# Performance work log

Measured on AMD Instinct MI355X. Metric: run time of the kernel, lower is better.

Reference implementation:

```python
import jax, jax.numpy as jnp
import numpy as np


def conv3d(x, w, b=None):
    # x: (N,C,D,H,W), w: (O,I,3,3,3), stride 1, padding 1 == SAME
    y = jax.lax.conv_general_dilated(x, w, (1, 1, 1), 'SAME',
                                     dimension_numbers=('NCDHW', 'OIDHW', 'NCDHW'))
    if b is not None:
        y = y + b[None, :, None, None, None]
    return y


def grid_sample_3d(vol, gx, gy, gz):
    # vol: (B,D,H,W); gx/gy/gz: normalized coords in [-1,1], shape (B,D,H,W)
    # trilinear, zeros padding, align_corners=True (old torch default)
    B, D, H, W = vol.shape
    ix = (gx + 1.0) * 0.5 * (W - 1)
    iy = (gy + 1.0) * 0.5 * (H - 1)
    iz = (gz + 1.0) * 0.5 * (D - 1)
    x0f, y0f, z0f = jnp.floor(ix), jnp.floor(iy), jnp.floor(iz)
    tx, ty, tz = ix - x0f, iy - y0f, iz - z0f
    x0 = x0f.astype(jnp.int32)
    y0 = y0f.astype(jnp.int32)
    z0 = z0f.astype(jnp.int32)
    vol_flat = vol.reshape(B, D * H * W)
    out = jnp.zeros_like(vol)
    for dz in (0, 1):
        for dy in (0, 1):
            for dx in (0, 1):
                xc, yc, zc = x0 + dx, y0 + dy, z0 + dz
                w = ((tx if dx else 1.0 - tx) * (ty if dy else 1.0 - ty)
                     * (tz if dz else 1.0 - tz))
                inb = ((xc >= 0) & (xc < W) & (yc >= 0) & (yc < H)
                       & (zc >= 0) & (zc < D))
                idx = ((jnp.clip(zc, 0, D - 1) * H + jnp.clip(yc, 0, H - 1)) * W
                       + jnp.clip(xc, 0, W - 1))
                val = jnp.take_along_axis(vol_flat, idx.reshape(B, -1), axis=1)
                val = val.reshape(B, D, H, W) * inb.astype(vol.dtype)
                out = out + w * val
    return out


def setup_inputs() -> dict:
    key = jax.random.key(0)
    k1, k2, k3, k4 = jax.random.split(key, 4)
    B, C, Cout, S = 2, 32, 64, 64
    x = jax.random.normal(k1, (B, C, S, S, S), dtype=jnp.float32)
    w_off = jax.random.normal(k2, (3 * C, C, 3, 3, 3), dtype=jnp.float32) * 0.0005
    w_reg = jax.random.normal(k3, (Cout, C, 3, 3, 3), dtype=jnp.float32) * 0.05
    b_reg = jax.random.normal(k4, (Cout,), dtype=jnp.float32) * 0.05
    return {"x": x, "w_off": w_off, "w_reg": w_reg, "b_reg": b_reg}


def reference(x, w_off, w_reg, b_reg):
    B, C, D, H, W = x.shape
    offset = conv3d(x, w_off)  # (B, 3C, D, H, W)
    off_w, off_h, _ = jnp.split(offset, 3, axis=1)
    # NOTE: original code has offset_d = offset_h (faithful bug)
    off_d = off_h
    off_w = off_w.reshape(B * C, D, H, W)
    off_h = off_h.reshape(B * C, D, H, W)
    off_d = off_d.reshape(B * C, D, H, W)
    # np.meshgrid default 'xy' indexing: shapes (H, W, D) -> requires D==H==W
    gw, gh, gd = np.meshgrid(np.linspace(-1, 1, W), np.linspace(-1, 1, H),
                             np.linspace(-1, 1, D))
    grid_w = jnp.asarray(gw, dtype=x.dtype)
    grid_h = jnp.asarray(gh, dtype=x.dtype)
    grid_d = jnp.asarray(gd, dtype=x.dtype)
    off_w = off_w + grid_w
    off_h = off_h + grid_h
    off_d = off_d + grid_d
    vol = x.reshape(B * C, D, H, W)
    # torch grid stack order: (offset_h, offset_w, offset_d) -> (x, y, z)
    sampled = grid_sample_3d(vol, off_h, off_w, off_d)
    sampled = sampled.reshape(B, C, D, H, W)
    return conv3d(sampled, w_reg, b_reg)
```

## Files before the change

kernel.cpp:

```cpp
#include <hip/hip_runtime.h>
#include <cstddef>

#define S 64
#define VOL (64*64*64)
#define CIN 32

typedef __attribute__((ext_vector_type(8))) short bf16x8;
typedef __attribute__((ext_vector_type(4))) float floatx4;

struct __attribute__((packed, aligned(4))) fpair { float x, y; };

__device__ __forceinline__ unsigned short f2bf(float f) {
    union { float f; unsigned u; } v; v.f = f;
    unsigned r = v.u + 0x7fffu + ((v.u >> 16) & 1u);
    return (unsigned short)(r >> 16);
}
__device__ __forceinline__ float bf2f(unsigned short h) {
    union { unsigned u; float f; } v; v.u = ((unsigned)h) << 16;
    return v.f;
}
__device__ __forceinline__ int iclamp(int v, int lo, int hi) {
    return v < lo ? lo : (v > hi ? hi : v);
}

__device__ __forceinline__ void load4bf(const float* p, unsigned short* o) {
    const float4 v = *(const float4*)p;
    o[0] = f2bf(v.x); o[1] = f2bf(v.y); o[2] = f2bf(v.z); o[3] = f2bf(v.w);
}
__device__ __forceinline__ void load4bf(const unsigned short* p, unsigned short* o) {
    const ushort4 v = *(const ushort4*)p;
    o[0] = v.x; o[1] = v.y; o[2] = v.z; o[3] = v.w;
}

__global__ void prep_w_kernel(const float* __restrict__ w_off,
                              const float* __restrict__ w_reg,
                              unsigned short* __restrict__ wt1,
                              unsigned short* __restrict__ wt2) {
    int i = blockIdx.x * 256 + threadIdx.x;
    if (i >= 27 * 64 * 32) return;
    int ci = i & 31;
    int co = (i >> 5) & 63;
    int tap = i >> 11;
    wt1[i] = f2bf(w_off[(co * 32 + ci) * 27 + tap]);
    wt2[i] = f2bf(w_reg[(co * 32 + ci) * 27 + tap]);
}

template <typename TIN, bool WRITE_OFF>
__global__ __launch_bounds__(256, 2)
void conv_mfma_kernel(const TIN* __restrict__ src,
                      const unsigned short* __restrict__ wt,
                      const float* __restrict__ bias,
                      void* __restrict__ dstv) {
    __shared__ unsigned short lds[16 * 64 * 32];

    const int d0 = blockIdx.x * 2;
    const int h0 = blockIdx.y * 2;
    const int b  = blockIdx.z;
    const int t  = threadIdx.x;

    const TIN* sb = src + (size_t)b * CIN * VOL;

    const int w0 = (t & 15) << 2;
    const int c0 = (t >> 4) << 1;
    const int jj = c0 >> 3;
    const int cb = (c0 & 7) << 1;
    const int sw01 = (w0 >> 1) & 3;
    const int sw23 = ((w0 >> 1) + 1) & 3;

#pragma unroll
    for (int rr = 0; rr < 16; ++rr) {
        const int z = d0 - 1 + (rr >> 2);
        const int y = h0 - 1 + (rr & 3);
        unsigned pk0 = 0, pk1 = 0, pk2 = 0, pk3 = 0;
        if (((unsigned)z < 64u) && ((unsigned)y < 64u)) {
            const TIN* p0 = sb + (size_t)c0 * VOL + (z * 64 + y) * 64 + w0;
            unsigned short va[4], vb[4];
            load4bf(p0, va);
            load4bf(p0 + VOL, vb);
            pk0 = (unsigned)va[0] | ((unsigned)vb[0] << 16);
            pk1 = (unsigned)va[1] | ((unsigned)vb[1] << 16);
            pk2 = (unsigned)va[2] | ((unsigned)vb[2] << 16);
            pk3 = (unsigned)va[3] | ((unsigned)vb[3] << 16);
        }
        char* rbase = (char*)lds + (rr << 12) + cb;
        *(unsigned*)(rbase + ((w0 + 0) << 6) + ((jj ^ sw01) << 4)) = pk0;
        *(unsigned*)(rbase + ((w0 + 1) << 6) + ((jj ^ sw01) << 4)) = pk1;
        *(unsigned*)(rbase + ((w0 + 2) << 6) + ((jj ^ sw23) << 4)) = pk2;
        *(unsigned*)(rbase + ((w0 + 3) << 6) + ((jj ^ sw23) << 4)) = pk3;
    }
    __syncthreads();

    const int lane = t & 63;
    const int wv   = t >> 6;
    const int r    = lane & 15;
    const int q    = lane >> 4;
    const int dd   = wv >> 1;
    const int hh   = wv & 1;

    int P[4][3];
#pragma unroll
    for (int nt = 0; nt < 4; ++nt)
#pragma unroll
        for (int kw = 0; kw < 3; ++kw) {
            const int s  = nt * 16 + r + kw - 1;
            const int sc = s & 63;
            P[nt][kw] = (sc << 6) + ((q ^ ((sc >> 1) & 3)) << 4);
        }

    floatx4 acc[4][4];
#pragma unroll
    for (int mt = 0; mt < 4; ++mt)
#pragma unroll
        for (int nt = 0; nt < 4; ++nt)
#pragma unroll
            for (int rg = 0; rg < 4; ++rg) acc[mt][nt][rg] = 0.f;

    const bf16x8 z8 = {0, 0, 0, 0, 0, 0, 0, 0};

#pragma unroll
    for (int tap = 0; tap < 27; ++tap) {
        const int kd = tap / 9;
        const int kh = (tap % 9) / 3;
        const int kw = tap % 3;
        const int rowb = ((((dd + kd) << 2) + hh + kh) << 12);

        bf16x8 afr[4];
#pragma unroll
        for (int mt = 0; mt < 4; ++mt)
            afr[mt] = *(const bf16x8*)&wt[tap * 2048 + (mt * 16 + r) * 32 + q * 8];

        bf16x8 bfr[4];
#pragma unroll
        for (int nt = 0; nt < 4; ++nt)
            bfr[nt] = *(const bf16x8*)((const char*)lds + rowb + P[nt][kw]);

        if (kw == 0) { if (r == 0)  bfr[0] = z8; }
        if (kw == 2) { if (r == 15) bfr[3] = z8; }

#pragma unroll
        for (int mt = 0; mt < 4; ++mt)
#pragma unroll
            for (int nt = 0; nt < 4; ++nt)
                acc[mt][nt] = __builtin_amdgcn_mfma_f32_16x16x32_bf16(
                                  afr[mt], bfr[nt], acc[mt][nt], 0, 0, 0);
    }

    const int dw = (d0 + dd) * 4096 + (h0 + hh) * 64;
    if (WRITE_OFF) {
#pragma unroll
        for (int mt = 0; mt < 2; ++mt) {
#pragma unroll
            for (int nt = 0; nt < 4; ++nt) {
#pragma unroll
                for (int rg = 0; rg < 4; ++rg) {
                    const int c   = mt * 16 + q * 4 + rg;
                    const int pos = dw + nt * 16 + r;
                    const unsigned pk = (unsigned)f2bf(acc[mt][nt][rg])
                                      | ((unsigned)f2bf(acc[mt + 2][nt][rg]) << 16);
                    ((unsigned*)dstv)[((size_t)(b * 32 + c)) * VOL + pos] = pk;
                }
            }
        }
    } else {
#pragma unroll
        for (int mt = 0; mt < 4; ++mt) {
#pragma unroll
            for (int nt = 0; nt < 4; ++nt) {
#pragma unroll
                for (int rg = 0; rg < 4; ++rg) {
                    const int co  = mt * 16 + q * 4 + rg;
                    const int pos = dw + nt * 16 + r;
                    ((float*)dstv)[((size_t)(b * 64 + co)) * VOL + pos]
                        = acc[mt][nt][rg] + bias[co];
                }
            }
        }
    }
}

__global__ __launch_bounds__(256)
void gather_kernel(const float* __restrict__ x,
                   const unsigned* __restrict__ off32,
                   unsigned short* __restrict__ sampled) {
    __shared__ unsigned ostage[16][17];
    __shared__ float res[16][17];

    const unsigned gid = blockIdx.x;
    const int xcd = gid & 7;
    const int j   = gid >> 3;
    const int v   = xcd + ((j >> 10) << 3);
    const int bx  = j & 1023;
    const int c   = v & 31;
    const int b   = v >> 5;
    const int wt4 = bx & 3;
    const int dt  = (bx >> 2) & 3;
    const int h   = bx >> 4;
    const int t   = threadIdx.x;

    {
        const int wA = t & 15, dA = t >> 4;
        ostage[dA][wA] = off32[((size_t)(b * 32 + c)) * VOL
                               + (dt * 16 + dA) * 4096 + h * 64 + wt4 * 16 + wA];
    }
    __syncthreads();

    const int d_i = t & 15;
    const int w_i = t >> 4;
    const int d = dt * 16 + d_i;
    const int w = wt4 * 16 + w_i;

    const unsigned ow = ostage[d_i][w_i];
    const float offw = bf2f((unsigned short)(ow & 0xffffu));
    const float offh = bf2f((unsigned short)(ow >> 16));

    const float* vol = x + ((size_t)(b * CIN + c)) * VOL;

    const float ix = offh * 31.5f + (float)d;
    const float iy = offw * 31.5f + (float)h;
    const float iz = offh * 31.5f + (float)w;

    const float x0f = floorf(ix), y0f = floorf(iy), z0f = floorf(iz);
    const float tx = ix - x0f, ty = iy - y0f, tz = iz - z0f;
    const int ix0 = (int)x0f, iy0 = (int)y0f, iz0 = (int)z0f;

    const int bx0 = iclamp(ix0, 0, 62);
    const bool sel = (ix0 == bx0);
    const float w0x = ((unsigned)ix0 < 64u)       ? (1.f - tx) : 0.f;
    const float w1x = ((unsigned)(ix0 + 1) < 64u) ? tx         : 0.f;

    float out = 0.f;
#pragma unroll
    for (int dz = 0; dz < 2; ++dz) {
        const int zc = iz0 + dz;
        const bool zok = ((unsigned)zc < 64u);
        const int zcc = iclamp(zc, 0, 63);
        const float wz = dz ? tz : 1.f - tz;
#pragma unroll
        for (int dy = 0; dy < 2; ++dy) {
            const int yc = iy0 + dy;
            const bool yok = ((unsigned)yc < 64u);
            const int ycc = iclamp(yc, 0, 63);
            const float wzy = (zok && yok) ? wz * (dy ? ty : 1.f - ty) : 0.f;

            const fpair vp = *(const fpair*)&vol[(zcc * 64 + ycc) * 64 + bx0];
            const float v0 = sel ? vp.x : vp.y;
            const float v1 = sel ? vp.y : vp.x;
            out += wzy * (w0x * v0 + w1x * v1);
        }
    }

    res[w_i][d_i] = out;
    __syncthreads();

    const int w_o = t & 15;
    const int d_o = t >> 4;
    sampled[((size_t)(b * CIN + c)) * VOL + (dt * 16 + d_o) * 4096 + h * 64
            + wt4 * 16 + w_o] = f2bf(res[w_o][d_o]);
}

extern "C" void kernel_launch(void* const* d_in, const int* in_sizes, int n_in,
                              void* d_out, int out_size, void* d_ws, size_t ws_size,
                              hipStream_t stream) {
    (void)in_sizes; (void)n_in; (void)out_size; (void)ws_size;
    const float* x     = (const float*)d_in[0];
    const float* w_off = (const float*)d_in[1];
    const float* w_reg = (const float*)d_in[2];
    const float* b_reg = (const float*)d_in[3];
    float* out = (float*)d_out;

    unsigned* off32         = (unsigned*)d_ws;
    unsigned short* sampled = (unsigned short*)(off32 + (size_t)2 * 32 * VOL);
    unsigned short* wt1     = sampled + (size_t)2 * CIN * VOL;
    unsigned short* wt2     = wt1 + 27 * 64 * 32;

    prep_w_kernel<<<216, 256, 0, stream>>>(w_off, w_reg, wt1, wt2);

    dim3 cgrid(32, 32, 2);
    conv_mfma_kernel<float, true><<<cgrid, 256, 0, stream>>>(x, wt1, nullptr, (void*)off32);

    gather_kernel<<<65536, 256, 0, stream>>>(x, off32, sampled);

    conv_mfma_kernel<unsigned short, false><<<cgrid, 256, 0, stream>>>(sampled, wt2, b_reg, (void*)out);
}
```

Before: 426.2 us.

## Switch intermediates to channel-last bf16 layout with direct global-to-LDS loads

Adds a prepack kernel that converts x into a channel-last bf16 buffer, so both convolutions stage their input tiles with global_load_lds 16-byte transfers instead of strided per-channel loads and in-register packing. The offset conv now writes its output channel-last with 16-byte stores. The gather kernel has each thread handle all 32 channels of one voxel, which removes its LDS transposes and lets the sampled buffer reuse the prepacked buffer. This adds an extra pass over x and puts a 32-float array per gather thread, which raises register pressure. The gather's random reads are no longer grouped by channel per block, so cache locality may get worse.

```diff
diff --git a/kernel.cpp b/kernel.cpp
--- a/kernel.cpp
+++ b/kernel.cpp
@@ -23,13 +23,10 @@
     return v < lo ? lo : (v > hi ? hi : v);
 }
 
-__device__ __forceinline__ void load4bf(const float* p, unsigned short* o) {
-    const float4 v = *(const float4*)p;
-    o[0] = f2bf(v.x); o[1] = f2bf(v.y); o[2] = f2bf(v.z); o[3] = f2bf(v.w);
-}
-__device__ __forceinline__ void load4bf(const unsigned short* p, unsigned short* o) {
-    const ushort4 v = *(const ushort4*)p;
-    o[0] = v.x; o[1] = v.y; o[2] = v.z; o[3] = v.w;
+__device__ __forceinline__ void gload_lds16(const void* g, void* l) {
+    __builtin_amdgcn_global_load_lds(
+        (const __attribute__((address_space(1))) void*)g,
+        (__attribute__((address_space(3))) void*)l, 16, 0, 0);
 }
 
 __global__ void prep_w_kernel(const float* __restrict__ w_off,
@@ -45,9 +42,30 @@
     wt2[i] = f2bf(w_reg[(co * 32 + ci) * 27 + tap]);
 }
 
-template <typename TIN, bool WRITE_OFF>
+__global__ __launch_bounds__(256)
+void prepack_kernel(const float* __restrict__ x, unsigned* __restrict__ xb) {
+    const unsigned id = blockIdx.x * 256 + threadIdx.x;
+    const int b   = id >> 18;
+    const int pos = id & (VOL - 1);
+    const float* sp = x + (size_t)b * 32 * VOL + pos;
+    float v[32];
+#pragma unroll
+    for (int c = 0; c < 32; ++c) v[c] = sp[(size_t)c * VOL];
+    unsigned* dp = xb + (size_t)id * 16;
+#pragma unroll
+    for (int i = 0; i < 4; ++i) {
+        uint4 pk;
+        pk.x = (unsigned)f2bf(v[i*8+0]) | ((unsigned)f2bf(v[i*8+1]) << 16);
+        pk.y = (unsigned)f2bf(v[i*8+2]) | ((unsigned)f2bf(v[i*8+3]) << 16);
+        pk.z = (unsigned)f2bf(v[i*8+4]) | ((unsigned)f2bf(v[i*8+5]) << 16);
+        pk.w = (unsigned)f2bf(v[i*8+6]) | ((unsigned)f2bf(v[i*8+7]) << 16);
+        *(uint4*)(dp + i*4) = pk;
+    }
+}
+
+template <bool WRITE_OFF>
 __global__ __launch_bounds__(256, 2)
-void conv_mfma_kernel(const TIN* __restrict__ src,
+void conv_mfma_kernel(const unsigned short* __restrict__ src,
                       const unsigned short* __restrict__ wt,
                       const float* __restrict__ bias,
                       void* __restrict__ dstv) {
@@ -57,41 +75,33 @@
     const int h0 = blockIdx.y * 2;
     const int b  = blockIdx.z;
     const int t  = threadIdx.x;
-
-    const TIN* sb = src + (size_t)b * CIN * VOL;
-
-    const int w0 = (t & 15) << 2;
-    const int c0 = (t >> 4) << 1;
-    const int jj = c0 >> 3;
-    const int cb = (c0 & 7) << 1;
-    const int sw01 = (w0 >> 1) & 3;
-    const int sw23 = ((w0 >> 1) + 1) & 3;
-
-#pragma unroll
-    for (int rr = 0; rr < 16; ++rr) {
-        const int z = d0 - 1 + (rr >> 2);
-        const int y = h0 - 1 + (rr & 3);
-        unsigned pk0 = 0, pk1 = 0, pk2 = 0, pk3 = 0;
-        if (((unsigned)z < 64u) && ((unsigned)y < 64u)) {
-            const TIN* p0 = sb + (size_t)c0 * VOL + (z * 64 + y) * 64 + w0;
-            unsigned short va[4], vb[4];
-            load4bf(p0, va);
-            load4bf(p0 + VOL, vb);
-            pk0 = (unsigned)va[0] | ((unsigned)vb[0] << 16);
-            pk1 = (unsigned)va[1] | ((unsigned)vb[1] << 16);
-            pk2 = (unsigned)va[2] | ((unsigned)vb[2] << 16);
-            pk3 = (unsigned)va[3] | ((unsigned)vb[3] << 16);
-        }
-        char* rbase = (char*)lds + (rr << 12) + cb;
-        *(unsigned*)(rbase + ((w0 + 0) << 6) + ((jj ^ sw01) << 4)) = pk0;
-        *(unsigned*)(rbase + ((w0 + 1) << 6) + ((jj ^ sw01) << 4)) = pk1;
-        *(unsigned*)(rbase + ((w0 + 2) << 6) + ((jj ^ sw23) << 4)) = pk2;
-        *(unsigned*)(rbase + ((w0 + 3) << 6) + ((jj ^ sw23) << 4)) = pk3;
-    }
-    __syncthreads();
-
     const int lane = t & 63;
     const int wv   = t >> 6;
+
+    const int sl = lane >> 2;
+    const int js = (lane & 3) ^ ((lane >> 3) & 3);
+    const char* sbase = (const char*)src + (size_t)b * VOL * 64;
+#pragma unroll
+    for (int rr2 = 0; rr2 < 4; ++rr2) {
+        const int rowi = (wv << 2) + rr2;
+        const int z = d0 - 1 + (rowi >> 2);
+        const int y = h0 - 1 + (rowi & 3);
+        char* ldsrow = (char*)lds + (rowi << 12);
+        if (((unsigned)z < 64u) && ((unsigned)y < 64u)) {
+            const char* gb = sbase + ((size_t)(z * 4096 + y * 64)) * 64
+                           + (sl << 6) + (js << 4);
+#pragma unroll
+            for (int k = 0; k < 4; ++k)
+                gload_lds16(gb + (k << 10), ldsrow + (k << 10));
+        } else {
+            const uint4 z4 = make_uint4(0, 0, 0, 0);
+#pragma unroll
+            for (int k = 0; k < 4; ++k)
+                *(uint4*)(ldsrow + (k << 10) + (lane << 4)) = z4;
+        }
+    }
+    __syncthreads();
+
     const int r    = lane & 15;
     const int q    = lane >> 4;
     const int dd   = wv >> 1;
@@ -147,18 +157,18 @@
 
     const int dw = (d0 + dd) * 4096 + (h0 + hh) * 64;
     if (WRITE_OFF) {
+        unsigned* dst = (unsigned*)dstv + (size_t)b * VOL * 32;
 #pragma unroll
         for (int mt = 0; mt < 2; ++mt) {
 #pragma unroll
             for (int nt = 0; nt < 4; ++nt) {
-#pragma unroll
-                for (int rg = 0; rg < 4; ++rg) {
-                    const int c   = mt * 16 + q * 4 + rg;
-                    const int pos = dw + nt * 16 + r;
-                    const unsigned pk = (unsigned)f2bf(acc[mt][nt][rg])
-                                      | ((unsigned)f2bf(acc[mt + 2][nt][rg]) << 16);
-                    ((unsigned*)dstv)[((size_t)(b * 32 + c)) * VOL + pos] = pk;
-                }
+                const int pos = dw + nt * 16 + r;
+                uint4 pk;
+                pk.x = (unsigned)f2bf(acc[mt][nt][0]) | ((unsigned)f2bf(acc[mt+2][nt][0]) << 16);
+                pk.y = (unsigned)f2bf(acc[mt][nt][1]) | ((unsigned)f2bf(acc[mt+2][nt][1]) << 16);
+                pk.z = (unsigned)f2bf(acc[mt][nt][2]) | ((unsigned)f2bf(acc[mt+2][nt][2]) << 16);
+                pk.w = (unsigned)f2bf(acc[mt][nt][3]) | ((unsigned)f2bf(acc[mt+2][nt][3]) << 16);
+                *(uint4*)(dst + (size_t)pos * 32 + mt * 16 + q * 4) = pk;
             }
         }
     } else {
@@ -178,84 +188,87 @@
     }
 }
 
-__global__ __launch_bounds__(256)
+__global__ __launch_bounds__(256, 4)
 void gather_kernel(const float* __restrict__ x,
                    const unsigned* __restrict__ off32,
-                   unsigned short* __restrict__ sampled) {
-    __shared__ unsigned ostage[16][17];
-    __shared__ float res[16][17];
-
+                   unsigned* __restrict__ sampled) {
+    const int t = threadIdx.x;
     const unsigned gid = blockIdx.x;
-    const int xcd = gid & 7;
-    const int j   = gid >> 3;
-    const int v   = xcd + ((j >> 10) << 3);
-    const int bx  = j & 1023;
-    const int c   = v & 31;
-    const int b   = v >> 5;
-    const int wt4 = bx & 3;
-    const int dt  = (bx >> 2) & 3;
-    const int h   = bx >> 4;
-    const int t   = threadIdx.x;
-
-    {
-        const int wA = t & 15, dA = t >> 4;
-        ostage[dA][wA] = off32[((size_t)(b * 32 + c)) * VOL
-                               + (dt * 16 + dA) * 4096 + h * 64 + wt4 * 16 + wA];
-    }
-    __syncthreads();
-
+    const int b   = gid >> 10;
+    const int j   = gid & 1023;
+    const int wt4 = j & 3;
+    const int dt  = (j >> 2) & 3;
+    const int h   = j >> 4;
     const int d_i = t & 15;
     const int w_i = t >> 4;
     const int d = dt * 16 + d_i;
     const int w = wt4 * 16 + w_i;
-
-    const unsigned ow = ostage[d_i][w_i];
-    const float offw = bf2f((unsigned short)(ow & 0xffffu));
-    const float offh = bf2f((unsigned short)(ow >> 16));
-
-    const float* vol = x + ((size_t)(b * CIN + c)) * VOL;
-
-    const float ix = offh * 31.5f + (float)d;
-    const float iy = offw * 31.5f + (float)h;
-    const float iz = offh * 31.5f + (float)w;
-
-    const float x0f = floorf(ix), y0f = floorf(iy), z0f = floorf(iz);
-    const float tx = ix - x0f, ty = iy - y0f, tz = iz - z0f;
-    const int ix0 = (int)x0f, iy0 = (int)y0f, iz0 = (int)z0f;
-
-    const int bx0 = iclamp(ix0, 0, 62);
-    const bool sel = (ix0 == bx0);
-    const float w0x = ((unsigned)ix0 < 64u)       ? (1.f - tx) : 0.f;
-    const float w1x = ((unsigned)(ix0 + 1) < 64u) ? tx         : 0.f;
-
-    float out = 0.f;
-#pragma unroll
-    for (int dz = 0; dz < 2; ++dz) {
-        const int zc = iz0 + dz;
-        const bool zok = ((unsigned)zc < 64u);
-        const int zcc = iclamp(zc, 0, 63);
-        const float wz = dz ? tz : 1.f - tz;
-#pragma unroll
-        for (int dy = 0; dy < 2; ++dy) {
-            const int yc = iy0 + dy;
-            const bool yok = ((unsigned)yc < 64u);
-            const int ycc = iclamp(yc, 0, 63);
-            const float wzy = (zok && yok) ? wz * (dy ? ty : 1.f - ty) : 0.f;
-
-            const fpair vp = *(const fpair*)&vol[(zcc * 64 + ycc) * 64 + bx0];
-            const float v0 = sel ? vp.x : vp.y;
-            const float v1 = sel ? vp.y : vp.x;
-            out += wzy * (w0x * v0 + w1x * v1);
-        }
-    }
-
-    res[w_i][d_i] = out;
-    __syncthreads();
-
-    const int w_o = t & 15;
-    const int d_o = t >> 4;
-    sampled[((size_t)(b * CIN + c)) * VOL + (dt * 16 + d_o) * 4096 + h * 64
-            + wt4 * 16 + w_o] = f2bf(res[w_o][d_o]);
+    const int p = d * 4096 + h * 64 + w;
+
+    const unsigned* op = off32 + ((size_t)(b * VOL + p)) * 32;
+    const float* xb_ = x + (size_t)b * 32 * VOL;
+    const float fd = (float)d, fh = (float)h, fw = (float)w;
+
+    float outv[32];
+#pragma unroll
+    for (int cq = 0; cq < 8; ++cq) {
+        const uint4 o4 = *(const uint4*)(op + cq * 4);
+        const unsigned oarr[4] = {o4.x, o4.y, o4.z, o4.w};
+#pragma unroll
+        for (int ce = 0; ce < 4; ++ce) {
+            const int c = cq * 4 + ce;
+            const unsigned ow = oarr[ce];
+            const float offw = bf2f((unsigned short)(ow & 0xffffu));
+            const float offh = bf2f((unsigned short)(ow >> 16));
+            const float* vol = xb_ + (size_t)c * VOL;
+
+            const float ix = offh * 31.5f + fd;
+            const float iy = offw * 31.5f + fh;
+            const float iz = offh * 31.5f + fw;
+
+            const float x0f = floorf(ix), y0f = floorf(iy), z0f = floorf(iz);
+            const float tx = ix - x0f, ty = iy - y0f, tz = iz - z0f;
+            const int ix0 = (int)x0f, iy0 = (int)y0f, iz0 = (int)z0f;
+
+            const int bx0 = iclamp(ix0, 0, 62);
+            const bool sel = (ix0 == bx0);
+            const float w0x = ((unsigned)ix0 < 64u)       ? (1.f - tx) : 0.f;
+            const float w1x = ((unsigned)(ix0 + 1) < 64u) ? tx         : 0.f;
+
+            float out = 0.f;
+#pragma unroll
+            for (int dz = 0; dz < 2; ++dz) {
+                const int zc = iz0 + dz;
+                const bool zok = ((unsigned)zc < 64u);
+                const int zcc = iclamp(zc, 0, 63);
+                const float wz = dz ? tz : 1.f - tz;
+#pragma unroll
+                for (int dy = 0; dy < 2; ++dy) {
+                    const int yc = iy0 + dy;
+                    const bool yok = ((unsigned)yc < 64u);
+                    const int ycc = iclamp(yc, 0, 63);
+                    const float wzy = (zok && yok) ? wz * (dy ? ty : 1.f - ty) : 0.f;
+
+                    const fpair vp = *(const fpair*)&vol[(zcc * 64 + ycc) * 64 + bx0];
+                    const float v0 = sel ? vp.x : vp.y;
+                    const float v1 = sel ? vp.y : vp.x;
+                    out += wzy * (w0x * v0 + w1x * v1);
+                }
+            }
+            outv[c] = out;
+        }
+    }
+
+    unsigned* sp = sampled + ((size_t)(b * VOL + p)) * 16;
+#pragma unroll
+    for (int i = 0; i < 4; ++i) {
+        uint4 pk;
+        pk.x = (unsigned)f2bf(outv[i*8+0]) | ((unsigned)f2bf(outv[i*8+1]) << 16);
+        pk.y = (unsigned)f2bf(outv[i*8+2]) | ((unsigned)f2bf(outv[i*8+3]) << 16);
+        pk.z = (unsigned)f2bf(outv[i*8+4]) | ((unsigned)f2bf(outv[i*8+5]) << 16);
+        pk.w = (unsigned)f2bf(outv[i*8+6]) | ((unsigned)f2bf(outv[i*8+7]) << 16);
+        *(uint4*)(sp + i*4) = pk;
+    }
 }
 
 extern "C" void kernel_launch(void* const* d_in, const int* in_sizes, int n_in,
@@ -268,17 +281,20 @@
     const float* b_reg = (const float*)d_in[3];
     float* out = (float*)d_out;
 
-    unsigned* off32         = (unsigned*)d_ws;
-    unsigned short* sampled = (unsigned short*)(off32 + (size_t)2 * 32 * VOL);
-    unsigned short* wt1     = sampled + (size_t)2 * CIN * VOL;
-    unsigned short* wt2     = wt1 + 27 * 64 * 32;
+    unsigned* off32 = (unsigned*)d_ws;
+    unsigned* buf   = off32 + (size_t)2 * VOL * 32;
+    unsigned short* wt1 = (unsigned short*)(buf + (size_t)2 * VOL * 16);
+    unsigned short* wt2 = wt1 + 27 * 64 * 32;
 
     prep_w_kernel<<<216, 256, 0, stream>>>(w_off, w_reg, wt1, wt2);
+    prepack_kernel<<<2048, 256, 0, stream>>>(x, buf);
 
     dim3 cgrid(32, 32, 2);
-    conv_mfma_kernel<float, true><<<cgrid, 256, 0, stream>>>(x, wt1, nullptr, (void*)off32);
-
-    gather_kernel<<<65536, 256, 0, stream>>>(x, off32, sampled);
-
-    conv_mfma_kernel<unsigned short, false><<<cgrid, 256, 0, stream>>>(sampled, wt2, b_reg, (void*)out);
-}
+    conv_mfma_kernel<true><<<cgrid, 256, 0, stream>>>(
+        (const unsigned short*)buf, wt1, nullptr, (void*)off32);
+
+    gather_kernel<<<2048, 256, 0, stream>>>(x, off32, buf);
+
+    conv_mfma_kernel<false><<<cgrid, 256, 0, stream>>>(
+        (const unsigned short*)buf, wt2, b_reg, (void*)out);
+}
```

Measured after the change: 445.8 us. 1.05x slower.
